# Optimization experiments

Measured on AMD Instinct MI355X. Metric: run time of the kernel, lower is better.

The kernel has to match this reference:

```python
import jax, jax.numpy as jnp
import numpy as np

B, P = 4, 50000
D_IN, COND = 3, 48
# layer l: in IN_DIMS[l] -> out OUT_DIMS[l]; dims=[3,256*8,257], skip at layer index 4
IN_DIMS  = [D_IN + COND, 256, 256, 256, 256, 256, 256, 256, 256]
OUT_DIMS = [256, 256, 256, 253, 256, 256, 256, 256, 257]
N_LIN = 9
INV_SQRT2 = np.float32(1.0 / np.sqrt(2.0))


def softplus_beta100(x):
    return jax.nn.softplus(100.0 * x) * 0.01


def setup_inputs() -> dict:
    key = jax.random.key(0)
    ks = jax.random.split(key, 2 + 2 * N_LIN)
    inp = {
        "input": jax.random.normal(ks[0], (B, P, D_IN), dtype=jnp.float32),
        "cond_pose": jax.random.normal(ks[1], (B, COND), dtype=jnp.float32),
    }
    for l in range(N_LIN):
        scale = np.float32(np.sqrt(2.0 / OUT_DIMS[l]))  # geometry-style init scale
        inp[f"W{l}"] = jax.random.normal(ks[2 + 2 * l], (OUT_DIMS[l], IN_DIMS[l]), dtype=jnp.float32) * scale
        inp[f"b{l}"] = jnp.zeros((OUT_DIMS[l],), dtype=jnp.float32)
    return inp


def reference(input, cond_pose,
              W0, b0, W1, b1, W2, b2, W3, b3, W4, b4, W5, b5, W6, b6, W7, b7, W8, b8):
    Ws = [W0, W1, W2, W3, W4, W5, W6, W7, W8]
    bs = [b0, b1, b2, b3, b4, b5, b6, b7, b8]
    nb, npnt, nd = input.shape
    x_in = input.reshape(nb * npnt, nd)                                   # (N, 3)
    c = jnp.broadcast_to(cond_pose[:, None, :], (nb, npnt, COND)).reshape(nb * npnt, COND)
    x = jnp.concatenate([x_in, c], axis=-1)                               # cond concat at layer 0
    for l in range(N_LIN):
        if l == 4:  # skip connection: concat raw input, scaled by 1/sqrt(2)
            x = jnp.concatenate([x, x_in], axis=-1) * INV_SQRT2
        x = x @ Ws[l].T + bs[l]
        if l < N_LIN - 1:
            x = softplus_beta100(x)
    return x.reshape(nb, npnt, -1)                                        # (B, P, 257)
```

## Files before the change

kernel.cpp:

```cpp
#include <hip/hip_runtime.h>


typedef __attribute__((ext_vector_type(8))) short bf16x8;
typedef __attribute__((ext_vector_type(4))) float f32x4;

#define PPTS 50000

__device__ __forceinline__ short f2bf(float f) {
    union { float f; unsigned u; } v; v.f = f;
    unsigned r = v.u + 0x7fffu + ((v.u >> 16) & 1u);
    return (short)(r >> 16);
}

__device__ __forceinline__ unsigned cvt_pk_bf16(float lo, float hi) {
    unsigned r;
    asm("v_cvt_pk_bf16_f32 %0, %1, %2" : "=v"(r) : "v"(lo), "v"(hi));
    return r;
}

__device__ __forceinline__ float softplus100(float x) {
    const float A = 6.9314718e-3f, B = -3.11522e-3f, C = 9.8829e-4f;
    float e = __builtin_amdgcn_exp2f(fabsf(x) * -144.26950408889634f);
    float t = __builtin_fmaf(C, e, B);
    t = __builtin_fmaf(t, e, A);
    return __builtin_fmaf(e, t, fmaxf(x, 0.0f));
}

__device__ __forceinline__ int xswz(int row) {
    return (((row & 7) ^ (5 * ((row >> 3) & 1))) << 4);
}
__device__ __forceinline__ short* xaddr(short* base, int row, int col) {
    int off = ((row << 9) + (col << 1)) ^ xswz(row);
    return (short*)((char*)base + off);
}
__device__ __forceinline__ const short* xaddrc(const short* base, int row, int col) {
    int off = ((row << 9) + (col << 1)) ^ xswz(row);
    return (const short*)((const char*)base + off);
}

__global__ void prep_kernel(
    const float* __restrict__ W0, const float* __restrict__ W1, const float* __restrict__ W2,
    const float* __restrict__ W3, const float* __restrict__ W4, const float* __restrict__ W5,
    const float* __restrict__ W6, const float* __restrict__ W7, const float* __restrict__ W8,
    short* __restrict__ wbf)
{
    const int gid = blockIdx.x * blockDim.x + threadIdx.x;
    if (gid >= 68096) return;
    int l, cid; const float* Wsrc;
    if      (gid <  2048) { l = 0; cid = gid;         Wsrc = W0; }
    else if (gid < 10240) { l = 1; cid = gid -  2048; Wsrc = W1; }
    else if (gid < 18432) { l = 2; cid = gid - 10240; Wsrc = W2; }
    else if (gid < 26624) { l = 3; cid = gid - 18432; Wsrc = W3; }
    else if (gid < 34816) { l = 4; cid = gid - 26624; Wsrc = W4; }
    else if (gid < 43008) { l = 5; cid = gid - 34816; Wsrc = W5; }
    else if (gid < 51200) { l = 6; cid = gid - 43008; Wsrc = W6; }
    else if (gid < 59392) { l = 7; cid = gid - 51200; Wsrc = W7; }
    else                  { l = 8; cid = gid - 59392; Wsrc = W8; }
    const int NR   = (l == 3) ? 253 : ((l == 8) ? 257 : 256);
    const int KR   = (l == 0) ? 51 : 256;
    const int klog = (l == 0) ? 1 : 3;
    const int lane  = cid & 63;
    const int tile  = cid >> 6;
    const int ntile = tile >> klog;
    const int ktile = tile & ((1 << klog) - 1);
    const int n  = ntile * 16 + (lane & 15);
    const int k0 = ktile * 32 + ((lane >> 4) << 3);
    bf16x8 v;
#pragma unroll
    for (int j = 0; j < 8; ++j) {
        int k = k0 + j;
        float f = (n < NR && k < KR) ? Wsrc[n * KR + k] : 0.0f;
        v[j] = f2bf(f);
    }
    ((bf16x8*)wbf)[gid] = v;
}

template<int KSTEPS, int MODE>
__device__ __forceinline__ void layer_fwd(short* xb,
    const bf16x8* __restrict__ wl, const float* __restrict__ bias, int lane, int wid)
{
    const int prow = lane & 15;
    const int kg   = (lane >> 4) << 3;
    const int rb4  = (lane >> 4) << 2;
    f32x4 acc[4][2] = {};
#pragma unroll 2
    for (int ks = 0; ks < KSTEPS; ++ks) {
        bf16x8 a[2], b[4];
#pragma unroll
        for (int nii = 0; nii < 2; ++nii)
            a[nii] = wl[((wid * 2 + nii) * KSTEPS + ks) * 64 + lane];
#pragma unroll
        for (int mi = 0; mi < 4; ++mi)
            b[mi] = *(const bf16x8*)xaddrc(xb, mi * 16 + prow, ks * 32 + kg);
#pragma unroll
        for (int mi = 0; mi < 4; ++mi)
#pragma unroll
            for (int nii = 0; nii < 2; ++nii)
                acc[mi][nii] = __builtin_amdgcn_mfma_f32_16x16x32_bf16(
                    a[nii], b[mi], acc[mi][nii], 0, 0, 0);
    }
    __syncthreads();
#pragma unroll
    for (int nii = 0; nii < 2; ++nii) {
        const int cb = (wid * 2 + nii) * 16 + rb4;
        f32x4 bv;
        if (MODE == 1 && cb == 252) { f32x4 tb = {bias[252], 0.f, 0.f, 0.f}; bv = tb; }
        else bv = *(const f32x4*)(bias + cb);
#pragma unroll
        for (int mi = 0; mi < 4; ++mi) {
            float s[4];
#pragma unroll
            for (int r = 0; r < 4; ++r) {
                float v = softplus100(acc[mi][nii][r] + bv[r]);
                if (MODE == 1) v *= 0.70710678f;
                s[r] = v;
            }
            unsigned p01 = cvt_pk_bf16(s[0], s[1]);
            unsigned p23 = cvt_pk_bf16(s[2], s[3]);
            if (MODE == 1 && cb == 252) {
                *xaddr(xb, mi * 16 + prow, 252) = (short)(p01 & 0xffff);
            } else {
                uint2 pk; pk.x = p01; pk.y = p23;
                *(uint2*)xaddr(xb, mi * 16 + prow, cb) = pk;
            }
        }
    }
}

__global__ __launch_bounds__(512, 6) void net_kernel(
    const float* __restrict__ xin, const float* __restrict__ cond,
    const bf16x8* __restrict__ W,
    const float* __restrict__ b0, const float* __restrict__ b1, const float* __restrict__ b2,
    const float* __restrict__ b3, const float* __restrict__ b4, const float* __restrict__ b5,
    const float* __restrict__ b6, const float* __restrict__ b7, const float* __restrict__ b8,
    float* __restrict__ out)
{
    __shared__ short xb[64 * 256];
    const int t    = threadIdx.x;
    const int pt0  = blockIdx.x * 64;
    const int lane = t & 63;
    const int wid  = t >> 6;

    float sk[3] = {0.f, 0.f, 0.f};
    if (t < 64) {
#pragma unroll
        for (int c = 0; c < 3; ++c)
            sk[c] = xin[(pt0 + t) * 3 + c] * 0.70710678f;
    }

    {
        const int row   = t >> 3;
        const int c0    = (t & 7) << 3;
        const int point = pt0 + row;
        const int batch = point / PPTS;
        const float* xp = xin + point * 3;
        const float* cp = cond + batch * 48;
        bf16x8 v;
#pragma unroll
        for (int i = 0; i < 8; ++i) {
            int c = c0 + i;
            float f = (c < 3) ? xp[c] : ((c < 51) ? cp[c - 3] : 0.0f);
            v[i] = f2bf(f);
        }
        *(bf16x8*)xaddr(xb, row, c0) = v;
    }
    __syncthreads();

    layer_fwd<2, 0>(xb, W +     0, b0, lane, wid); __syncthreads();
    layer_fwd<8, 0>(xb, W +  2048, b1, lane, wid); __syncthreads();
    layer_fwd<8, 0>(xb, W + 10240, b2, lane, wid); __syncthreads();
    layer_fwd<8, 1>(xb, W + 18432, b3, lane, wid);
    if (t < 64) {
#pragma unroll
        for (int c = 0; c < 3; ++c)
            *xaddr(xb, t, 253 + c) = f2bf(sk[c]);
    }
    __syncthreads();
    layer_fwd<8, 0>(xb, W + 26624, b4, lane, wid); __syncthreads();
    layer_fwd<8, 0>(xb, W + 34816, b5, lane, wid); __syncthreads();
    layer_fwd<8, 0>(xb, W + 43008, b6, lane, wid); __syncthreads();
    layer_fwd<8, 0>(xb, W + 51200, b7, lane, wid); __syncthreads();

    {
        const bf16x8* wl = W + 59392;
        const int prow = lane & 15;
        const int kg   = (lane >> 4) << 3;
        const int rb4  = (lane >> 4) << 2;
#pragma unroll
        for (int half = 0; half < 2; ++half) {
            f32x4 acc[2][2] = {};
            f32x4 acc2[2]   = {};
#pragma unroll 2
            for (int ks = 0; ks < 8; ++ks) {
                bf16x8 a[2], b[2], a2;
#pragma unroll
                for (int nii = 0; nii < 2; ++nii)
                    a[nii] = wl[((wid * 2 + nii) * 8 + ks) * 64 + lane];
                if (wid == 0) a2 = wl[(128 + ks) * 64 + lane];
#pragma unroll
                for (int m2 = 0; m2 < 2; ++m2)
                    b[m2] = *(const bf16x8*)xaddrc(xb, (half * 2 + m2) * 16 + prow,
                                                   ks * 32 + kg);
#pragma unroll
                for (int m2 = 0; m2 < 2; ++m2) {
#pragma unroll
                    for (int nii = 0; nii < 2; ++nii)
                        acc[m2][nii] = __builtin_amdgcn_mfma_f32_16x16x32_bf16(
                            a[nii], b[m2], acc[m2][nii], 0, 0, 0);
                }
                if (wid == 0) {
#pragma unroll
                    for (int m2 = 0; m2 < 2; ++m2)
                        acc2[m2] = __builtin_amdgcn_mfma_f32_16x16x32_bf16(
                            a2, b[m2], acc2[m2], 0, 0, 0);
                }
            }
#pragma unroll
            for (int nii = 0; nii < 2; ++nii) {
                const int cb = (wid * 2 + nii) * 16 + rb4;
                const f32x4 bv = *(const f32x4*)(b8 + cb);
#pragma unroll
                for (int m2 = 0; m2 < 2; ++m2) {
                    const int rowoff = (pt0 + (half * 2 + m2) * 16 + prow) * 257 + cb;
#pragma unroll
                    for (int r = 0; r < 4; ++r)
                        out[rowoff + r] = acc[m2][nii][r] + bv[r];
                }
            }
            if (wid == 0 && rb4 == 0) {
                const float blast = b8[256];
#pragma unroll
                for (int m2 = 0; m2 < 2; ++m2)
                    out[(pt0 + (half * 2 + m2) * 16 + prow) * 257 + 256]
                        = acc2[m2][0] + blast;
            }
        }
    }
}

extern "C" void kernel_launch(void* const* d_in, const int* in_sizes, int n_in,
                              void* d_out, int out_size, void* d_ws, size_t ws_size,
                              hipStream_t stream)
{
    const float* xin  = (const float*)d_in[0];
    const float* cond = (const float*)d_in[1];
    const float* Wp[9]; const float* bp[9];
    for (int l = 0; l < 9; ++l) { Wp[l] = (const float*)d_in[2 + 2 * l]; bp[l] = (const float*)d_in[3 + 2 * l]; }
    short* wbf = (short*)d_ws;

    prep_kernel<<<dim3(266), dim3(256), 0, stream>>>(
        Wp[0], Wp[1], Wp[2], Wp[3], Wp[4], Wp[5], Wp[6], Wp[7], Wp[8], wbf);
    net_kernel<<<dim3(3125), dim3(512), 0, stream>>>(
        xin, cond, (const bf16x8*)wbf,
        bp[0], bp[1], bp[2], bp[3], bp[4], bp[5], bp[6], bp[7], bp[8],
        (float*)d_out);
}
```

Before: 305.2 us.

## Widen per-wave output tiles, halve block size, fold skip scale into weights

Each wave now computes four 16-column output tiles instead of two, and blocks shrink from 512 to 256 threads (4 waves). This halves the redundant LDS reads of the activation tile per block and raises MFMA work per loaded operand. The skip-connection 1/sqrt(2) is folded into layer-4 weights during prep instead of being applied to activations. The softplus epilogue is computed before the barrier into registers, using paired float math, so it can overlap with other waves finishing their GEMMs. The risk is lower occupancy, since LDS per block is unchanged while each block has half as many waves, and higher register pressure from the larger accumulators.

Result: slower. 321.6 us (+5.4%).

```diff
diff --git a/kernel.cpp b/kernel.cpp
--- a/kernel.cpp
+++ b/kernel.cpp
@@ -3,6 +3,7 @@
 
 typedef __attribute__((ext_vector_type(8))) short bf16x8;
 typedef __attribute__((ext_vector_type(4))) float f32x4;
+typedef __attribute__((ext_vector_type(2))) float f32x2;
 
 #define PPTS 50000
 
@@ -18,12 +19,17 @@
     return r;
 }
 
-__device__ __forceinline__ float softplus100(float x) {
-    const float A = 6.9314718e-3f, B = -3.11522e-3f, C = 9.8829e-4f;
-    float e = __builtin_amdgcn_exp2f(fabsf(x) * -144.26950408889634f);
-    float t = __builtin_fmaf(C, e, B);
-    t = __builtin_fmaf(t, e, A);
-    return __builtin_fmaf(e, t, fmaxf(x, 0.0f));
+__device__ __forceinline__ f32x2 sp100_pair(f32x2 y) {
+    const f32x2 A2 = {6.9314718e-3f, 6.9314718e-3f};
+    const f32x2 B2 = {-3.11522e-3f, -3.11522e-3f};
+    const f32x2 C2 = {9.8829e-4f,  9.8829e-4f};
+    const f32x2 K2 = {-144.26950408889634f, -144.26950408889634f};
+    const f32x2 Z2 = {0.0f, 0.0f};
+    f32x2 m = __builtin_elementwise_abs(y) * K2;
+    f32x2 e = {__builtin_amdgcn_exp2f(m.x), __builtin_amdgcn_exp2f(m.y)};
+    f32x2 t = __builtin_elementwise_fma(C2, e, B2);
+    t = __builtin_elementwise_fma(t, e, A2);
+    return __builtin_elementwise_fma(e, t, __builtin_elementwise_max(y, Z2));
 }
 
 __device__ __forceinline__ int xswz(int row) {
@@ -59,6 +65,7 @@
     const int NR   = (l == 3) ? 253 : ((l == 8) ? 257 : 256);
     const int KR   = (l == 0) ? 51 : 256;
     const int klog = (l == 0) ? 1 : 3;
+    const float sc = (l == 4) ? 0.70710678f : 1.0f;
     const int lane  = cid & 63;
     const int tile  = cid >> 6;
     const int ntile = tile >> klog;
@@ -69,7 +76,7 @@
 #pragma unroll
     for (int j = 0; j < 8; ++j) {
         int k = k0 + j;
-        float f = (n < NR && k < KR) ? Wsrc[n * KR + k] : 0.0f;
+        float f = (n < NR && k < KR) ? Wsrc[n * KR + k] * sc : 0.0f;
         v[j] = f2bf(f);
     }
     ((bf16x8*)wbf)[gid] = v;
@@ -82,52 +89,55 @@
     const int prow = lane & 15;
     const int kg   = (lane >> 4) << 3;
     const int rb4  = (lane >> 4) << 2;
-    f32x4 acc[4][2] = {};
+    f32x4 acc[4][4] = {};
 #pragma unroll 2
     for (int ks = 0; ks < KSTEPS; ++ks) {
-        bf16x8 a[2], b[4];
-#pragma unroll
-        for (int nii = 0; nii < 2; ++nii)
-            a[nii] = wl[((wid * 2 + nii) * KSTEPS + ks) * 64 + lane];
+        bf16x8 a[4], b[4];
+#pragma unroll
+        for (int nii = 0; nii < 4; ++nii)
+            a[nii] = wl[((wid * 4 + nii) * KSTEPS + ks) * 64 + lane];
 #pragma unroll
         for (int mi = 0; mi < 4; ++mi)
             b[mi] = *(const bf16x8*)xaddrc(xb, mi * 16 + prow, ks * 32 + kg);
 #pragma unroll
         for (int mi = 0; mi < 4; ++mi)
 #pragma unroll
-            for (int nii = 0; nii < 2; ++nii)
+            for (int nii = 0; nii < 4; ++nii)
                 acc[mi][nii] = __builtin_amdgcn_mfma_f32_16x16x32_bf16(
                     a[nii], b[mi], acc[mi][nii], 0, 0, 0);
     }
-    __syncthreads();
-#pragma unroll
-    for (int nii = 0; nii < 2; ++nii) {
-        const int cb = (wid * 2 + nii) * 16 + rb4;
+    uint2 pk[4][4];
+#pragma unroll
+    for (int nii = 0; nii < 4; ++nii) {
+        const int cb = (wid * 4 + nii) * 16 + rb4;
         f32x4 bv;
         if (MODE == 1 && cb == 252) { f32x4 tb = {bias[252], 0.f, 0.f, 0.f}; bv = tb; }
         else bv = *(const f32x4*)(bias + cb);
 #pragma unroll
         for (int mi = 0; mi < 4; ++mi) {
-            float s[4];
-#pragma unroll
-            for (int r = 0; r < 4; ++r) {
-                float v = softplus100(acc[mi][nii][r] + bv[r]);
-                if (MODE == 1) v *= 0.70710678f;
-                s[r] = v;
-            }
-            unsigned p01 = cvt_pk_bf16(s[0], s[1]);
-            unsigned p23 = cvt_pk_bf16(s[2], s[3]);
-            if (MODE == 1 && cb == 252) {
-                *xaddr(xb, mi * 16 + prow, 252) = (short)(p01 & 0xffff);
-            } else {
-                uint2 pk; pk.x = p01; pk.y = p23;
-                *(uint2*)xaddr(xb, mi * 16 + prow, cb) = pk;
-            }
-        }
-    }
-}
-
-__global__ __launch_bounds__(512, 6) void net_kernel(
+            f32x2 y0 = {acc[mi][nii][0] + bv[0], acc[mi][nii][1] + bv[1]};
+            f32x2 y1 = {acc[mi][nii][2] + bv[2], acc[mi][nii][3] + bv[3]};
+            f32x2 r0 = sp100_pair(y0);
+            f32x2 r1 = sp100_pair(y1);
+            pk[nii][mi].x = cvt_pk_bf16(r0.x, r0.y);
+            pk[nii][mi].y = cvt_pk_bf16(r1.x, r1.y);
+        }
+    }
+    __syncthreads();
+#pragma unroll
+    for (int nii = 0; nii < 4; ++nii) {
+        const int cb = (wid * 4 + nii) * 16 + rb4;
+#pragma unroll
+        for (int mi = 0; mi < 4; ++mi) {
+            if (MODE == 1 && cb == 252)
+                *xaddr(xb, mi * 16 + prow, 252) = (short)(pk[nii][mi].x & 0xffff);
+            else
+                *(uint2*)xaddr(xb, mi * 16 + prow, cb) = pk[nii][mi];
+        }
+    }
+}
+
+__global__ __launch_bounds__(256, 4) void net_kernel(
     const float* __restrict__ xin, const float* __restrict__ cond,
     const bf16x8* __restrict__ W,
     const float* __restrict__ b0, const float* __restrict__ b1, const float* __restrict__ b2,
@@ -145,24 +155,27 @@
     if (t < 64) {
 #pragma unroll
         for (int c = 0; c < 3; ++c)
-            sk[c] = xin[(pt0 + t) * 3 + c] * 0.70710678f;
+            sk[c] = xin[(pt0 + t) * 3 + c];
     }
 
     {
-        const int row   = t >> 3;
-        const int c0    = (t & 7) << 3;
+        const int row   = t >> 2;
+        const int c0    = (t & 3) << 4;
         const int point = pt0 + row;
         const int batch = point / PPTS;
         const float* xp = xin + point * 3;
         const float* cp = cond + batch * 48;
-        bf16x8 v;
-#pragma unroll
-        for (int i = 0; i < 8; ++i) {
-            int c = c0 + i;
-            float f = (c < 3) ? xp[c] : ((c < 51) ? cp[c - 3] : 0.0f);
-            v[i] = f2bf(f);
-        }
-        *(bf16x8*)xaddr(xb, row, c0) = v;
+#pragma unroll
+        for (int h = 0; h < 2; ++h) {
+            bf16x8 v;
+#pragma unroll
+            for (int i = 0; i < 8; ++i) {
+                int c = c0 + h * 8 + i;
+                float f = (c < 3) ? xp[c] : ((c < 51) ? cp[c - 3] : 0.0f);
+                v[i] = f2bf(f);
+            }
+            *(bf16x8*)xaddr(xb, row, c0 + h * 8) = v;
+        }
     }
     __syncthreads();
 
@@ -188,26 +201,25 @@
         const int rb4  = (lane >> 4) << 2;
 #pragma unroll
         for (int half = 0; half < 2; ++half) {
-            f32x4 acc[2][2] = {};
+            f32x4 acc[2][4] = {};
             f32x4 acc2[2]   = {};
 #pragma unroll 2
             for (int ks = 0; ks < 8; ++ks) {
-                bf16x8 a[2], b[2], a2;
-#pragma unroll
-                for (int nii = 0; nii < 2; ++nii)
-                    a[nii] = wl[((wid * 2 + nii) * 8 + ks) * 64 + lane];
+                bf16x8 a[4], b[2], a2;
+#pragma unroll
+                for (int nii = 0; nii < 4; ++nii)
+                    a[nii] = wl[((wid * 4 + nii) * 8 + ks) * 64 + lane];
                 if (wid == 0) a2 = wl[(128 + ks) * 64 + lane];
 #pragma unroll
                 for (int m2 = 0; m2 < 2; ++m2)
                     b[m2] = *(const bf16x8*)xaddrc(xb, (half * 2 + m2) * 16 + prow,
                                                    ks * 32 + kg);
 #pragma unroll
-                for (int m2 = 0; m2 < 2; ++m2) {
-#pragma unroll
-                    for (int nii = 0; nii < 2; ++nii)
+                for (int m2 = 0; m2 < 2; ++m2)
+#pragma unroll
+                    for (int nii = 0; nii < 4; ++nii)
                         acc[m2][nii] = __builtin_amdgcn_mfma_f32_16x16x32_bf16(
                             a[nii], b[m2], acc[m2][nii], 0, 0, 0);
-                }
                 if (wid == 0) {
 #pragma unroll
                     for (int m2 = 0; m2 < 2; ++m2)
@@ -216,8 +228,8 @@
                 }
             }
 #pragma unroll
-            for (int nii = 0; nii < 2; ++nii) {
-                const int cb = (wid * 2 + nii) * 16 + rb4;
+            for (int nii = 0; nii < 4; ++nii) {
+                const int cb = (wid * 4 + nii) * 16 + rb4;
                 const f32x4 bv = *(const f32x4*)(b8 + cb);
 #pragma unroll
                 for (int m2 = 0; m2 < 2; ++m2) {
@@ -250,7 +262,7 @@
 
     prep_kernel<<<dim3(266), dim3(256), 0, stream>>>(
         Wp[0], Wp[1], Wp[2], Wp[3], Wp[4], Wp[5], Wp[6], Wp[7], Wp[8], wbf);
-    net_kernel<<<dim3(3125), dim3(512), 0, stream>>>(
+    net_kernel<<<dim3(3125), dim3(256), 0, stream>>>(
         xin, cond, (const bf16x8*)wbf,
         bp[0], bp[1], bp[2], bp[3], bp[4], bp[5], bp[6], bp[7], bp[8],
         (float*)d_out);
```
